# Kernel tuning notes

Hardware: AMD Instinct MI355X
Metric: run time of the kernel (lower is better)

The kernel has to match this reference:

```python
import jax, jax.numpy as jnp
import numpy as np

N, E = 100000, 1600000
DIMS = [128, 64, 64, 64, 32]  # in, hid, hid, hid, out
NEG_SLOPE = 0.2               # GATv2Conv default negative_slope
ELU_ALPHA_OUT = float(DIMS[-1])  # nn.ELU(out_channels): alpha = out_channels


def setup_inputs() -> dict:
    key = jax.random.key(0)
    ks = jax.random.split(key, 16)
    inp = {
        "x": jax.random.normal(ks[0], (N, DIMS[0]), dtype=jnp.float32),
        "edge_index": jax.random.randint(ks[1], (2, E), 0, N, dtype=jnp.int64),
    }
    ki = 2
    for i in range(4):
        fin, fout = DIMS[i], DIMS[i + 1]
        s = 1.0 / np.sqrt(fin)
        inp[f"Wl{i+1}"] = jax.random.uniform(ks[ki], (fin, fout), jnp.float32, -s, s); ki += 1
        inp[f"Wr{i+1}"] = jax.random.uniform(ks[ki], (fin, fout), jnp.float32, -s, s); ki += 1
        inp[f"att{i+1}"] = jax.random.uniform(ks[ki], (fout,), jnp.float32, -s, s); ki += 1
    return inp


def gatv2_layer(x, src, dst, Wl, Wr, att):
    # single head, concat=False, no self-loops, no bias (per module config)
    xl = x @ Wl                                   # [N, F] source-side projection
    xr = x @ Wr                                   # [N, F] target-side projection
    e = jax.nn.leaky_relu(xl[src] + xr[dst], NEG_SLOPE)   # [E, F]
    score = e @ att                               # [E]
    # softmax over incoming edges of each destination node
    m = jax.ops.segment_max(score, dst, num_segments=N)    # [N]
    ex = jnp.exp(score - m[dst])                  # [E]
    denom = jax.ops.segment_sum(ex, dst, num_segments=N)   # [N]
    alpha = ex / (denom[dst] + 1e-16)             # [E]
    # scatter-add weighted source messages
    return jax.ops.segment_sum(xl[src] * alpha[:, None], dst, num_segments=N)


def reference(x, edge_index, Wl1, Wr1, att1, Wl2, Wr2, att2, Wl3, Wr3, att3, Wl4, Wr4, att4):
    src, dst = edge_index[0], edge_index[1]
    h = jax.nn.elu(gatv2_layer(x, src, dst, Wl1, Wr1, att1))
    h = jax.nn.elu(gatv2_layer(h, src, dst, Wl2, Wr2, att2))
    h = jax.nn.elu(gatv2_layer(h, src, dst, Wl3, Wr3, att3))
    h = gatv2_layer(h, src, dst, Wl4, Wr4, att4)
    # nn.ELU(out_channels) -> ELU with alpha = out_channels (faithful quirk)
    return jnp.where(h > 0, h, ELU_ALPHA_OUT * jnp.expm1(h))
```

## Files before the change

### kernel.cpp

```cpp
#include <hip/hip_runtime.h>
#include <math.h>

typedef __attribute__((ext_vector_type(8))) short bf16x8;
typedef __attribute__((ext_vector_type(4))) float f32x4;
typedef __attribute__((ext_vector_type(2))) _Float16 h2;

#define BSHIFT 7
#define CH 8192

__device__ inline unsigned short f32_to_bf16_bits(float f) {
    unsigned int u = __float_as_uint(f);
    unsigned int r = (u + 0x7fffu + ((u >> 16) & 1u)) >> 16;
    return (unsigned short)r;
}
__device__ inline float bf16_bits_to_f32(unsigned short h) {
    return __uint_as_float(((unsigned int)h) << 16);
}
__device__ inline h2 u2h(unsigned u) { return __builtin_bit_cast(h2, u); }
__device__ inline unsigned h2u(h2 h) { return __builtin_bit_cast(unsigned, h); }

#define SWZ_ADD(t, imm) \
    t += __int_as_float(__builtin_amdgcn_ds_swizzle(__float_as_int(t), imm))

__device__ inline float dot2acc(h2 a, h2 b, float c) {
#if defined(__has_builtin)
#if __has_builtin(__builtin_amdgcn_fdot2)
    return __builtin_amdgcn_fdot2(a, b, c, false);
#else
    return c + (float)a[0] * (float)b[0] + (float)a[1] * (float)b[1];
#endif
#else
    return c + (float)a[0] * (float)b[0] + (float)a[1] * (float)b[1];
#endif
}


__global__ __launch_bounds__(256) void bucket_hist(
    const int* __restrict__ dst, int* __restrict__ bcnt8, int E, int nb, int nbp)
{
    __shared__ int h[1024];
    for (int i = threadIdx.x; i < nb; i += 256) h[i] = 0;
    __syncthreads();
    int e0 = blockIdx.x * CH, e1 = min(e0 + CH, E);
    for (int e = e0 + (int)threadIdx.x; e < e1; e += 256)
        atomicAdd(&h[dst[e] >> BSHIFT], 1);
    __syncthreads();
    int* mycnt = bcnt8 + (blockIdx.x & 7) * nbp;
    for (int b = threadIdx.x; b < nb; b += 256) {
        int c = h[b];
        if (c) atomicAdd(&mycnt[b], c);
    }
}

__global__ void bucket_scan(const int* __restrict__ bcnt8, int* __restrict__ bbase,
                            int* __restrict__ bcur8, int* __restrict__ rowstart,
                            int nb, int nbp, int E, int N)
{
    __shared__ int sh[1024];
    int t = threadIdx.x;
    int g8[8];
    int tot = 0;
#pragma unroll
    for (int g = 0; g < 8; ++g) {
        int c = (t < nb) ? bcnt8[g * nbp + t] : 0;
        g8[g] = c; tot += c;
    }
    sh[t] = tot;
    __syncthreads();
    for (int d = 1; d < 1024; d <<= 1) {
        int a = (t >= d) ? sh[t - d] : 0;
        __syncthreads();
        sh[t] += a;
        __syncthreads();
    }
    int base = sh[t] - tot;
    if (t <= nb) bbase[t] = base;
    if (t < nb) {
        int run = base;
#pragma unroll
        for (int g = 0; g < 8; ++g) { bcur8[g * nbp + t] = run; run += g8[g]; }
    }
    if (t == 0) rowstart[N] = E;
}

__global__ __launch_bounds__(256) void bucket_scatter(
    const int* __restrict__ src, const int* __restrict__ dst,
    int* __restrict__ bcur8, unsigned* __restrict__ pairs, int E, int nb, int nbp)
{
    __shared__ int h[1024];
    for (int i = threadIdx.x; i < nb; i += 256) h[i] = 0;
    __syncthreads();
    int e0 = blockIdx.x * CH, e1 = min(e0 + CH, E);
    for (int e = e0 + (int)threadIdx.x; e < e1; e += 256)
        atomicAdd(&h[dst[e] >> BSHIFT], 1);
    __syncthreads();
    int* mycur = bcur8 + (blockIdx.x & 7) * nbp;
    for (int b = threadIdx.x; b < nb; b += 256) {
        int c = h[b];
        if (c) h[b] = atomicAdd(&mycur[b], c);
    }
    __syncthreads();
    for (int e = e0 + (int)threadIdx.x; e < e1; e += 256) {
        int d = dst[e];
        int pos = atomicAdd(&h[d >> BSHIFT], 1);
        pairs[pos] = ((unsigned)src[e] << BSHIFT) | (unsigned)(d & 127);
    }
}

__global__ __launch_bounds__(256) void bucket_finalize(
    const unsigned* __restrict__ pairs, const int* __restrict__ bbase,
    int* __restrict__ rowstart, int* __restrict__ csr_src, int N)
{
    __shared__ int h[128];
    __shared__ int sh[256];
    int b = blockIdx.x;
    int p0 = bbase[b], p1 = bbase[b + 1];
    int t = threadIdx.x;
    if (t < 128) h[t] = 0;
    __syncthreads();
    for (int e = p0 + t; e < p1; e += 256)
        atomicAdd(&h[pairs[e] & 127], 1);
    __syncthreads();
    int v = (t < 128) ? h[t] : 0;
    sh[t] = v;
    __syncthreads();
    for (int d = 1; d < 256; d <<= 1) {
        int a = (t >= d) ? sh[t - d] : 0;
        __syncthreads();
        sh[t] += a;
        __syncthreads();
    }
    if (t < 128) {
        int off = sh[t] - v;
        int node = (b << BSHIFT) + t;
        if (node < N) rowstart[node] = p0 + off;
        h[t] = p0 + off;
    }
    __syncthreads();
    for (int e = p0 + t; e < p1; e += 256) {
        unsigned pr = pairs[e];
        int pos = atomicAdd(&h[pr & 127], 1);
        csr_src[pos] = (int)(pr >> BSHIFT);
    }
}


__device__ inline void prepack_one(const float* __restrict__ W, unsigned short* __restrict__ P,
                                   int FIN, int FOUT, int ii) {
    int NT = FOUT >> 4, NK = FIN >> 5;
    int part = NT * NK * 512;
    int j = ii & 7;
    int lane = (ii >> 3) & 63;
    int rest = ii >> 9;
    int ks = rest % NK;
    int t = rest / NK;
    int k = ks * 32 + (lane >> 4) * 8 + j;
    int c = t * 16 + (lane & 15);
    float w = W[(size_t)k * FOUT + c];
    unsigned short hi = f32_to_bf16_bits(w);
    unsigned short lo = f32_to_bf16_bits(w - bf16_bits_to_f32(hi));
    P[ii] = hi;
    P[part + ii] = lo;
}

__global__ void prepack_all(
    const float* Wl1, const float* Wr1, const float* Wl2, const float* Wr2,
    const float* Wl3, const float* Wr3, const float* Wl4, const float* Wr4,
    unsigned short* pWl1, unsigned short* pWr1, unsigned short* pWl2, unsigned short* pWr2,
    unsigned short* pWl3, unsigned short* pWr3, unsigned short* pWl4, unsigned short* pWr4)
{
    int i = blockIdx.x * 256 + threadIdx.x;
    if      (i < 8192)  prepack_one(Wl1, pWl1, 128, 64, i);
    else if (i < 16384) prepack_one(Wr1, pWr1, 128, 64, i - 8192);
    else if (i < 20480) prepack_one(Wl2, pWl2, 64, 64, i - 16384);
    else if (i < 24576) prepack_one(Wr2, pWr2, 64, 64, i - 20480);
    else if (i < 28672) prepack_one(Wl3, pWl3, 64, 64, i - 24576);
    else if (i < 32768) prepack_one(Wr3, pWr3, 64, 64, i - 28672);
    else if (i < 34816) prepack_one(Wl4, pWl4, 64, 32, i - 32768);
    else if (i < 36864) prepack_one(Wr4, pWr4, 64, 32, i - 34816);
}


template<int FIN, int FOUT, bool IN16>
__global__ __launch_bounds__(256) void proj_mfma_kernel(
    const void* __restrict__ xin,
    const unsigned short* __restrict__ pWl, const unsigned short* __restrict__ pWr,
    const float* __restrict__ att,
    _Float16* __restrict__ xlh, _Float16* __restrict__ xrh,
    float* __restrict__ dl, float* __restrict__ dr, int n)
{
    constexpr int NT = FOUT >> 4;
    constexpr int NK = FIN >> 5;
    constexpr int PART = NT * NK * 512;
    const int wave = threadIdx.x >> 6;
    const int lane = threadIdx.x & 63;
    const int row0 = blockIdx.x * 64 + wave * 16;
    int arow = row0 + (lane & 15);
    if (arow >= n) arow = n - 1;
    const int khalf = lane >> 4;

    f32x4 accl[NT], accr[NT];
#pragma unroll
    for (int t = 0; t < NT; ++t) {
        accl[t] = (f32x4){0.f, 0.f, 0.f, 0.f};
        accr[t] = (f32x4){0.f, 0.f, 0.f, 0.f};
    }

#pragma unroll
    for (int ks = 0; ks < NK; ++ks) {
        float av[8];
        if (IN16) {
            const _Float16* xrow = (const _Float16*)xin + (size_t)arow * FIN + khalf * 8;
            float4 raw = *(const float4*)(xrow + ks * 32);
            const unsigned* u = (const unsigned*)&raw;
#pragma unroll
            for (int j = 0; j < 4; ++j) {
                h2 p = u2h(u[j]);
                av[2 * j]     = (float)p[0];
                av[2 * j + 1] = (float)p[1];
            }
        } else {
            const float* xrow = (const float*)xin + (size_t)arow * FIN + khalf * 8;
            float4 a0 = *(const float4*)(xrow + ks * 32);
            float4 a1 = *(const float4*)(xrow + ks * 32 + 4);
            av[0] = a0.x; av[1] = a0.y; av[2] = a0.z; av[3] = a0.w;
            av[4] = a1.x; av[5] = a1.y; av[6] = a1.z; av[7] = a1.w;
        }
        bf16x8 ah, al;
#pragma unroll
        for (int j = 0; j < 8; ++j) {
            unsigned short h = f32_to_bf16_bits(av[j]);
            ah[j] = (short)h;
            al[j] = (short)f32_to_bf16_bits(av[j] - bf16_bits_to_f32(h));
        }
#pragma unroll
        for (int t = 0; t < NT; ++t) {
            const unsigned short* bpl = pWl + ((size_t)(t * NK + ks) * 64 + lane) * 8;
            bf16x8 bh  = *(const bf16x8*)bpl;
            bf16x8 blo = *(const bf16x8*)(bpl + PART);
            accl[t] = __builtin_amdgcn_mfma_f32_16x16x32_bf16(ah, bh,  accl[t], 0, 0, 0);
            accl[t] = __builtin_amdgcn_mfma_f32_16x16x32_bf16(ah, blo, accl[t], 0, 0, 0);
            accl[t] = __builtin_amdgcn_mfma_f32_16x16x32_bf16(al, bh,  accl[t], 0, 0, 0);
            const unsigned short* bpr = pWr + ((size_t)(t * NK + ks) * 64 + lane) * 8;
            bh  = *(const bf16x8*)bpr;
            blo = *(const bf16x8*)(bpr + PART);
            accr[t] = __builtin_amdgcn_mfma_f32_16x16x32_bf16(ah, bh,  accr[t], 0, 0, 0);
            accr[t] = __builtin_amdgcn_mfma_f32_16x16x32_bf16(ah, blo, accr[t], 0, 0, 0);
            accr[t] = __builtin_amdgcn_mfma_f32_16x16x32_bf16(al, bh,  accr[t], 0, 0, 0);
        }
    }

    const int orow0 = row0 + khalf * 4;
    const int colb = lane & 15;
    float attc[NT];
#pragma unroll
    for (int t = 0; t < NT; ++t) attc[t] = att[t * 16 + colb];

#pragma unroll
    for (int t = 0; t < NT; ++t) {
        int col = t * 16 + colb;
#pragma unroll
        for (int r = 0; r < 4; ++r) {
            int rr = orow0 + r;
            if (rr < n) {
                xlh[(size_t)rr * FOUT + col] = (_Float16)accl[t][r];
                xrh[(size_t)rr * FOUT + col] = (_Float16)accr[t][r];
            }
        }
    }
#pragma unroll
    for (int r = 0; r < 4; ++r) {
        float pl = 0.f, pr = 0.f;
#pragma unroll
        for (int t = 0; t < NT; ++t) { pl += accl[t][r] * attc[t]; pr += accr[t][r] * attc[t]; }
#pragma unroll
        for (int off = 1; off < 16; off <<= 1) {
            pl += __shfl_xor(pl, off);
            pr += __shfl_xor(pr, off);
        }
        int rr = orow0 + r;
        if (colb == 0 && rr < n) { dl[rr] = pl; dr[rr] = pr; }
    }
}


template<int F, int AMODE, bool OUT16>
__global__ __launch_bounds__(256) void agg_kernel(
    const _Float16* __restrict__ xlh, const _Float16* __restrict__ xrh,
    const float* __restrict__ att,
    const float* __restrict__ dl, const float* __restrict__ dr,
    const int* __restrict__ rowstart, const int* __restrict__ csr_src,
    void* __restrict__ outv, int n, int E, int ntiles)
{
    constexpr int LPE = F / 8;
    constexpr int LSH = (F == 64) ? 6 : 5;
    constexpr int NPG = 64 / LPE;

    int wv0  = (blockIdx.x * blockDim.x + threadIdx.x) >> 6;
    int nwaves = gridDim.x * (blockDim.x >> 6);
    int lane = threadIdx.x & 63;
    int grp = lane / LPE;
    int fl  = lane % LPE;

    h2 atth[4];
#pragma unroll
    for (int j = 0; j < 4; ++j) {
        atth[j][0] = (_Float16)att[fl * 8 + 2 * j];
        atth[j][1] = (_Float16)att[fl * 8 + 2 * j + 1];
    }

    for (int tile = wv0; tile < ntiles; tile += nwaves) {
        int node = tile * NPG + grp;
        bool act = node < n;
        int nc = act ? node : 0;

        float4 xrraw = *(const float4*)(xrh + (((unsigned)nc << LSH) + fl * 8));
        h2 xrv[4];
#pragma unroll
        for (int j = 0; j < 4; ++j) xrv[j] = u2h(((const unsigned*)&xrraw)[j]);
        float cdr = 0.6f * dr[nc];

        int s0 = rowstart[nc];
        int s1 = act ? rowstart[nc + 1] : s0;

        float m = -1e30f, mth = -1e30f, ssum = 0.f;
        float o[8];
#pragma unroll
        for (int j = 0; j < 8; ++j) o[j] = 0.f;

        int cA0 = csr_src[s0];
        int cB0 = csr_src[s0 + 1];
        int cA1 = csr_src[s0 + 2];
        int cB1 = csr_src[s0 + 3];
        float4 rA0 = *(const float4*)(xlh + (((unsigned)cA0 << LSH) + fl * 8));
        float4 rB0 = *(const float4*)(xlh + (((unsigned)cB0 << LSH) + fl * 8));
        float  dA0 = dl[cA0], dB0 = dl[cB0];
        float4 rA1 = *(const float4*)(xlh + (((unsigned)cA1 << LSH) + fl * 8));
        float4 rB1 = *(const float4*)(xlh + (((unsigned)cB1 << LSH) + fl * 8));
        float  dA1 = dl[cA1], dB1 = dl[cB1];
        int fA0 = csr_src[s0 + 4];
        int fB0 = csr_src[s0 + 5];
        int fA1 = csr_src[s0 + 6];
        int fB1 = csr_src[s0 + 7];

        int i0 = s0;

#define AGG_COMPUTE(RA, RB, DA, DB)                                          \
        {                                                                    \
            h2 a[4], b[4];                                                   \
            _Pragma("unroll")                                                \
            for (int j = 0; j < 4; ++j) {                                    \
                a[j] = u2h(((const unsigned*)&RA)[j]);                       \
                b[j] = u2h(((const unsigned*)&RB)[j]);                       \
            }                                                                \
            bool vb = (i0 + 1) < s1;                                         \
            float ta = 0.f, tb = 0.f;                                        \
            _Pragma("unroll")                                                \
            for (int j = 0; j < 4; ++j) {                                    \
                h2 ea = a[j] + xrv[j];                                       \
                h2 eb = b[j] + xrv[j];                                       \
                ea = u2h(h2u(ea) & 0x7FFF7FFFu);                             \
                eb = u2h(h2u(eb) & 0x7FFF7FFFu);                             \
                ta = dot2acc(atth[j], ea, ta);                               \
                tb = dot2acc(atth[j], eb, tb);                               \
            }                                                                \
            SWZ_ADD(ta, 0x041F); SWZ_ADD(tb, 0x041F);                        \
            SWZ_ADD(ta, 0x081F); SWZ_ADD(tb, 0x081F);                        \
            if (LPE == 8) { SWZ_ADD(ta, 0x101F); SWZ_ADD(tb, 0x101F); }      \
            float pa = 0.6f * DA + cdr + 0.4f * ta;                          \
            float pb = vb ? (0.6f * DB + cdr + 0.4f * tb) : -1e30f;          \
            float pm = fmaxf(pa, pb);                                        \
            if (pm > mth) {                                                  \
                float c = __expf(m - pm);                                    \
                ssum *= c;                                                   \
                _Pragma("unroll")                                            \
                for (int j = 0; j < 8; ++j) o[j] *= c;                       \
                m = pm; mth = pm + 8.0f;                                     \
            }                                                                \
            float wa = __expf(pa - m);                                       \
            float wb = __expf(pb - m);                                       \
            ssum += wa + wb;                                                 \
            _Pragma("unroll")                                                \
            for (int j = 0; j < 4; ++j) {                                    \
                o[2 * j]     += wa * (float)a[j][0] + wb * (float)b[j][0];   \
                o[2 * j + 1] += wa * (float)a[j][1] + wb * (float)b[j][1];   \
            }                                                                \
        }

        while (i0 < s1) {
            {
                int cA2 = fA0, cB2 = fB0;
                fA0 = csr_src[i0 + 8];
                fB0 = csr_src[i0 + 9];
                AGG_COMPUTE(rA0, rB0, dA0, dB0);
                rA0 = *(const float4*)(xlh + (((unsigned)cA2 << LSH) + fl * 8));
                rB0 = *(const float4*)(xlh + (((unsigned)cB2 << LSH) + fl * 8));
                dA0 = dl[cA2]; dB0 = dl[cB2];
            }
            i0 += 2;
            if (i0 >= s1) break;
            {
                int cA2 = fA1, cB2 = fB1;
                fA1 = csr_src[i0 + 8];
                fB1 = csr_src[i0 + 9];
                AGG_COMPUTE(rA1, rB1, dA1, dB1);
                rA1 = *(const float4*)(xlh + (((unsigned)cA2 << LSH) + fl * 8));
                rB1 = *(const float4*)(xlh + (((unsigned)cB2 << LSH) + fl * 8));
                dA1 = dl[cA2]; dB1 = dl[cB2];
            }
            i0 += 2;
        }
#undef AGG_COMPUTE

        float inv = 1.f / (ssum + 1e-16f);
        float res[8];
#pragma unroll
        for (int j = 0; j < 8; ++j) {
            float r = o[j] * inv;
            if (AMODE == 1) r = (r > 0.f) ? r : expm1f(r);
            else            r = (r > 0.f) ? r : 32.f * expm1f(r);
            res[j] = r;
        }
        if (act) {
            if (OUT16) {
                unsigned pk[4];
#pragma unroll
                for (int j = 0; j < 4; ++j) {
                    h2 t;
                    t[0] = (_Float16)res[2 * j];
                    t[1] = (_Float16)res[2 * j + 1];
                    pk[j] = h2u(t);
                }
                _Float16* op = (_Float16*)outv + (((unsigned)node << LSH) + fl * 8);
                *(float4*)op = *(const float4*)pk;
            } else {
                float* op = (float*)outv + (((unsigned)node << LSH) + fl * 8);
                *(float4*)op       = (float4){res[0], res[1], res[2], res[3]};
                *(float4*)(op + 4) = (float4){res[4], res[5], res[6], res[7]};
            }
        }
    }
}


extern "C" void kernel_launch(void* const* d_in, const int* in_sizes, int n_in,
                              void* d_out, int out_size, void* d_ws, size_t ws_size,
                              hipStream_t stream) {
    const float* x    = (const float*)d_in[0];
    const int*   ei   = (const int*)d_in[1];
    const float* Wl1  = (const float*)d_in[2];
    const float* Wr1  = (const float*)d_in[3];
    const float* att1 = (const float*)d_in[4];
    const float* Wl2  = (const float*)d_in[5];
    const float* Wr2  = (const float*)d_in[6];
    const float* att2 = (const float*)d_in[7];
    const float* Wl3  = (const float*)d_in[8];
    const float* Wr3  = (const float*)d_in[9];
    const float* att3 = (const float*)d_in[10];
    const float* Wl4  = (const float*)d_in[11];
    const float* Wr4  = (const float*)d_in[12];
    const float* att4 = (const float*)d_in[13];

    const int N = in_sizes[0] / 128;
    const int E = in_sizes[1] / 2;
    const int* src = ei;
    const int* dst = ei + E;

    const int nb  = (N + 127) >> BSHIFT;
    const int nbp = (nb + 15) & ~15;

    char* w = (char*)d_ws;
    size_t off = 0;
    auto take = [&](size_t bytes) -> void* {
        void* p = w + off;
        off = (off + bytes + 255) & ~(size_t)255;
        return p;
    };
    int* bcnt8    = (int*)take((size_t)8 * nbp * 4);
    int* bcur8    = (int*)take((size_t)8 * nbp * 4);
    int* bbase    = (int*)take((size_t)(nb + 1) * 4);
    int* rowstart = (int*)take((size_t)(N + 1) * 4);
    int* csr_src  = (int*)take((size_t)(E + 16) * 4);
    float* dl = (float*)take((size_t)N * 4);
    float* dr = (float*)take((size_t)N * 4);
    _Float16* xlh = (_Float16*)take((size_t)N * 64 * 2);
    _Float16* xrh = (_Float16*)take((size_t)N * 64 * 2);
    _Float16* hA  = (_Float16*)take((size_t)N * 64 * 2);
    _Float16* hB  = (_Float16*)take((size_t)N * 64 * 2);
    unsigned short* pWl1 = (unsigned short*)take(2 * 4 * 4 * 512 * 2);
    unsigned short* pWr1 = (unsigned short*)take(2 * 4 * 4 * 512 * 2);
    unsigned short* pWl2 = (unsigned short*)take(2 * 4 * 2 * 512 * 2);
    unsigned short* pWr2 = (unsigned short*)take(2 * 4 * 2 * 512 * 2);
    unsigned short* pWl3 = (unsigned short*)take(2 * 4 * 2 * 512 * 2);
    unsigned short* pWr3 = (unsigned short*)take(2 * 4 * 2 * 512 * 2);
    unsigned short* pWl4 = (unsigned short*)take(2 * 2 * 2 * 512 * 2);
    unsigned short* pWr4 = (unsigned short*)take(2 * 2 * 2 * 512 * 2);
    unsigned* pairs = (unsigned*)hA;
    float* outf = (float*)d_out;

    hipMemsetAsync(bcnt8, 0, (size_t)8 * nbp * 4, stream);
    hipMemsetAsync(csr_src + E, 0, 16 * 4, stream);

    prepack_all<<<144, 256, 0, stream>>>(Wl1, Wr1, Wl2, Wr2, Wl3, Wr3, Wl4, Wr4,
                                         pWl1, pWr1, pWl2, pWr2, pWl3, pWr3, pWl4, pWr4);

    int kgrid = (E + CH - 1) / CH;
    bucket_hist<<<kgrid, 256, 0, stream>>>(dst, bcnt8, E, nb, nbp);
    bucket_scan<<<1, 1024, 0, stream>>>(bcnt8, bbase, bcur8, rowstart, nb, nbp, E, N);
    bucket_scatter<<<kgrid, 256, 0, stream>>>(src, dst, bcur8, pairs, E, nb, nbp);
    bucket_finalize<<<nb, 256, 0, stream>>>(pairs, bbase, rowstart, csr_src, N);

    int pblk = (N + 63) / 64;
    const int AGGB = 2048;
    int nt64 = (N + 7) / 8;
    int nt32 = (N + 15) / 16;

    proj_mfma_kernel<128, 64, false><<<pblk, 256, 0, stream>>>(x, pWl1, pWr1, att1, xlh, xrh, dl, dr, N);
    agg_kernel<64, 1, true><<<AGGB, 256, 0, stream>>>(xlh, xrh, att1, dl, dr, rowstart, csr_src, hA, N, E, nt64);

    proj_mfma_kernel<64, 64, true><<<pblk, 256, 0, stream>>>(hA, pWl2, pWr2, att2, xlh, xrh, dl, dr, N);
    agg_kernel<64, 1, true><<<AGGB, 256, 0, stream>>>(xlh, xrh, att2, dl, dr, rowstart, csr_src, hB, N, E, nt64);

    proj_mfma_kernel<64, 64, true><<<pblk, 256, 0, stream>>>(hB, pWl3, pWr3, att3, xlh, xrh, dl, dr, N);
    agg_kernel<64, 1, true><<<AGGB, 256, 0, stream>>>(xlh, xrh, att3, dl, dr, rowstart, csr_src, hA, N, E, nt64);

    proj_mfma_kernel<64, 32, true><<<pblk, 256, 0, stream>>>(hA, pWl4, pWr4, att4, xlh, xrh, dl, dr, N);
    agg_kernel<32, 2, false><<<AGGB, 256, 0, stream>>>(xlh, xrh, att4, dl, dr, rowstart, csr_src, outf, N, E, nt32);
}
```

Baseline: 291.0 us.

## Store per-block bucket histograms and scan them instead of recounting in scatter

The bucket sort now writes each block's local histogram to global memory. A single-block scan turns these into exclusive per-block offsets, and the scatter kernel reads those offsets directly, so it no longer recomputes the histogram or does global atomics. This removes a second pass over dst, the 8-way atomic counters and a memset. In exchange the one-block scan walks kgrid (~196) rows serially per bucket, which may be slow.

```diff
diff --git a/kernel.cpp b/kernel.cpp
--- a/kernel.cpp
+++ b/kernel.cpp
@@ -36,7 +36,7 @@
 
 
 __global__ __launch_bounds__(256) void bucket_hist(
-    const int* __restrict__ dst, int* __restrict__ bcnt8, int E, int nb, int nbp)
+    const int* __restrict__ dst, int* __restrict__ bh, int E, int nb, int nbp)
 {
     __shared__ int h[1024];
     for (int i = threadIdx.x; i < nb; i += 256) h[i] = 0;
@@ -45,27 +45,26 @@
     for (int e = e0 + (int)threadIdx.x; e < e1; e += 256)
         atomicAdd(&h[dst[e] >> BSHIFT], 1);
     __syncthreads();
-    int* mycnt = bcnt8 + (blockIdx.x & 7) * nbp;
-    for (int b = threadIdx.x; b < nb; b += 256) {
-        int c = h[b];
-        if (c) atomicAdd(&mycnt[b], c);
-    }
-}
-
-__global__ void bucket_scan(const int* __restrict__ bcnt8, int* __restrict__ bbase,
-                            int* __restrict__ bcur8, int* __restrict__ rowstart,
-                            int nb, int nbp, int E, int N)
+    for (int b = threadIdx.x; b < nb; b += 256)
+        bh[(size_t)blockIdx.x * nbp + b] = h[b];
+}
+
+__global__ void bucket_scan(int* __restrict__ bh, int* __restrict__ bbase,
+                            int* __restrict__ rowstart,
+                            int nb, int nbp, int kgrid, int E, int N)
 {
     __shared__ int sh[1024];
     int t = threadIdx.x;
-    int g8[8];
-    int tot = 0;
-#pragma unroll
-    for (int g = 0; g < 8; ++g) {
-        int c = (t < nb) ? bcnt8[g * nbp + t] : 0;
-        g8[g] = c; tot += c;
-    }
-    sh[t] = tot;
+    int run = 0;
+    if (t < nb) {
+        for (int b = 0; b < kgrid; ++b) {
+            int* p = &bh[(size_t)b * nbp + t];
+            int v = *p;
+            *p = run;
+            run += v;
+        }
+    }
+    sh[t] = run;
     __syncthreads();
     for (int d = 1; d < 1024; d <<= 1) {
         int a = (t >= d) ? sh[t - d] : 0;
@@ -73,36 +72,27 @@
         sh[t] += a;
         __syncthreads();
     }
-    int base = sh[t] - tot;
-    if (t <= nb) bbase[t] = base;
+    int base = sh[t] - run;
     if (t < nb) {
-        int run = base;
-#pragma unroll
-        for (int g = 0; g < 8; ++g) { bcur8[g * nbp + t] = run; run += g8[g]; }
-    }
+        bbase[t] = base;
+        for (int b = 0; b < kgrid; ++b) bh[(size_t)b * nbp + t] += base;
+    }
+    if (t == nb) bbase[t] = E;
     if (t == 0) rowstart[N] = E;
 }
 
 __global__ __launch_bounds__(256) void bucket_scatter(
     const int* __restrict__ src, const int* __restrict__ dst,
-    int* __restrict__ bcur8, unsigned* __restrict__ pairs, int E, int nb, int nbp)
-{
-    __shared__ int h[1024];
-    for (int i = threadIdx.x; i < nb; i += 256) h[i] = 0;
+    const int* __restrict__ bh, unsigned* __restrict__ pairs, int E, int nb, int nbp)
+{
+    __shared__ int cur[1024];
+    for (int i = threadIdx.x; i < nb; i += 256)
+        cur[i] = bh[(size_t)blockIdx.x * nbp + i];
     __syncthreads();
     int e0 = blockIdx.x * CH, e1 = min(e0 + CH, E);
-    for (int e = e0 + (int)threadIdx.x; e < e1; e += 256)
-        atomicAdd(&h[dst[e] >> BSHIFT], 1);
-    __syncthreads();
-    int* mycur = bcur8 + (blockIdx.x & 7) * nbp;
-    for (int b = threadIdx.x; b < nb; b += 256) {
-        int c = h[b];
-        if (c) h[b] = atomicAdd(&mycur[b], c);
-    }
-    __syncthreads();
     for (int e = e0 + (int)threadIdx.x; e < e1; e += 256) {
         int d = dst[e];
-        int pos = atomicAdd(&h[d >> BSHIFT], 1);
+        int pos = atomicAdd(&cur[d >> BSHIFT], 1);
         pairs[pos] = ((unsigned)src[e] << BSHIFT) | (unsigned)(d & 127);
     }
 }
@@ -468,6 +458,7 @@
 
     const int nb  = (N + 127) >> BSHIFT;
     const int nbp = (nb + 15) & ~15;
+    const int kgrid = (E + CH - 1) / CH;
 
     char* w = (char*)d_ws;
     size_t off = 0;
@@ -476,8 +467,7 @@
         off = (off + bytes + 255) & ~(size_t)255;
         return p;
     };
-    int* bcnt8    = (int*)take((size_t)8 * nbp * 4);
-    int* bcur8    = (int*)take((size_t)8 * nbp * 4);
+    int* bh       = (int*)take((size_t)kgrid * nbp * 4);
     int* bbase    = (int*)take((size_t)(nb + 1) * 4);
     int* rowstart = (int*)take((size_t)(N + 1) * 4);
     int* csr_src  = (int*)take((size_t)(E + 16) * 4);
@@ -498,16 +488,14 @@
     unsigned* pairs = (unsigned*)hA;
     float* outf = (float*)d_out;
 
-    hipMemsetAsync(bcnt8, 0, (size_t)8 * nbp * 4, stream);
     hipMemsetAsync(csr_src + E, 0, 16 * 4, stream);
 
     prepack_all<<<144, 256, 0, stream>>>(Wl1, Wr1, Wl2, Wr2, Wl3, Wr3, Wl4, Wr4,
                                          pWl1, pWr1, pWl2, pWr2, pWl3, pWr3, pWl4, pWr4);
 
-    int kgrid = (E + CH - 1) / CH;
-    bucket_hist<<<kgrid, 256, 0, stream>>>(dst, bcnt8, E, nb, nbp);
-    bucket_scan<<<1, 1024, 0, stream>>>(bcnt8, bbase, bcur8, rowstart, nb, nbp, E, N);
-    bucket_scatter<<<kgrid, 256, 0, stream>>>(src, dst, bcur8, pairs, E, nb, nbp);
+    bucket_hist<<<kgrid, 256, 0, stream>>>(dst, bh, E, nb, nbp);
+    bucket_scan<<<1, 1024, 0, stream>>>(bh, bbase, rowstart, nb, nbp, kgrid, E, N);
+    bucket_scatter<<<kgrid, 256, 0, stream>>>(src, dst, bh, pairs, E, nb, nbp);
     bucket_finalize<<<nb, 256, 0, stream>>>(pairs, bbase, rowstart, csr_src, N);
 
     int pblk = (N + 63) / 64;
```

Measured after the change: 357.0 us. 22.7% more time.
